# Kernel tuning notes

Measured on AMD Instinct MI355X. Metric: run time of the kernel, lower is better.

The kernel has to match this reference:

```python
import jax, jax.numpy as jnp
import numpy as np

EPS = 1e-6

def gram_schmidt_orthonormalize(U, eps=EPS):
    # U: [B, K, D] -> orthonormalized along K, vectorized over batch
    B, K, D = U.shape
    vs = []
    for i in range(K):
        v = U[:, i]  # [B, D]
        for vj in vs:
            coeff = jnp.sum(v * vj, axis=1, keepdims=True) / (jnp.sum(vj * vj, axis=1, keepdims=True) + eps)
            v = v - coeff * vj
        norm = jnp.maximum(jnp.linalg.norm(v, axis=1, keepdims=True), eps)
        vs.append(v / norm)
    return jnp.stack(vs, axis=1)  # [B, K, D]

def setup_inputs() -> dict:
    key = jax.random.key(0)
    ks = jax.random.split(key, 14)
    B, IN, H1, H2, OUT, E, G = 4096, 1024, 2048, 2048, 512, 8, 256
    s = 0.02
    return {
        "x":   jax.random.normal(ks[0], (B, IN), jnp.float32),
        "W1":  jax.random.normal(ks[1], (E, IN, H1), jnp.float32) * s,
        "b1":  jnp.zeros((E, H1), jnp.float32),
        "W2":  jax.random.normal(ks[2], (E, H1, H2), jnp.float32) * s,
        "b2":  jnp.zeros((E, H2), jnp.float32),
        "W3":  jax.random.normal(ks[3], (E, H2, OUT), jnp.float32) * s,
        "b3":  jnp.zeros((E, OUT), jnp.float32),
        "Wg1": jax.random.normal(ks[4], (IN, G), jnp.float32) * s,
        "bg1": jnp.zeros((G,), jnp.float32),
        "Wg2": jax.random.normal(ks[5], (G, E), jnp.float32) * s,
        "bg2": jnp.zeros((E,), jnp.float32),
        "Wo":  jax.random.normal(ks[6], (OUT, 1), jnp.float32) * s,
        "bo":  jnp.zeros((1,), jnp.float32),
    }

def reference(x, W1, b1, W2, b2, W3, b3, Wg1, bg1, Wg2, bg2, Wo, bo):
    # Expert MLPs, batched over expert axis e: [B,E,h]
    h = jax.nn.relu(jnp.einsum('bi,eih->beh', x, W1) + b1)
    h = jax.nn.relu(jnp.einsum('beh,ehk->bek', h, W2) + b2)
    expert_outputs = jnp.einsum('bek,ekd->bed', h, W3) + b3  # [B, E, D]
    # Gating network: MLP + softmax over experts
    g = jax.nn.relu(x @ Wg1 + bg1)
    gate_weights = jax.nn.softmax(g @ Wg2 + bg2, axis=-1)  # [B, E]
    # Per-sample Gram-Schmidt across experts, weighted combine
    ortho = gram_schmidt_orthonormalize(expert_outputs)  # [B, E, D]
    combined = jnp.einsum('bed,be->bd', ortho, gate_weights)  # [B, D]
    final = combined @ Wo + bo  # [B, 1]
    return (final, 0.0)
```

## Files before the change

### kernel.cpp

```cpp
#include <hip/hip_runtime.h>
#include <hip/hip_bf16.h>

#define DEVINL __device__ __forceinline__

constexpr int Bsz = 4096, INF = 1024, H1 = 2048, H2 = 2048, OUTD = 512, NE = 8, G = 256;

typedef __attribute__((ext_vector_type(8))) short bf16x8;
typedef __attribute__((ext_vector_type(16))) float f32x16;

typedef unsigned short u16;

DEVINL u16 f2bf(float f) {
  unsigned int u = __float_as_uint(f);
  u = (u + 0x7FFFu + ((u >> 16) & 1u)) >> 16;
  return (u16)u;
}
DEVINL float bf2f(u16 h) { return __uint_as_float((unsigned int)h << 16); }

DEVINL void gload16(const void* g, void* l) {
  __builtin_amdgcn_global_load_lds(
      (const __attribute__((address_space(1))) void*)g,
      (__attribute__((address_space(3))) void*)l, 16, 0, 0);
}

DEVINL float waveAllSum(float v) {
#pragma unroll
  for (int m = 32; m > 0; m >>= 1) v += __shfl_xor(v, m, 64);
  return v;
}

DEVINL f32x16 mfma3(bf16x8 bh, bf16x8 bl, bf16x8 ah, bf16x8 al, f32x16 c) {
  c = __builtin_amdgcn_mfma_f32_32x32x16_bf16(bh, ah, c, 0, 0, 0);
  c = __builtin_amdgcn_mfma_f32_32x32x16_bf16(bl, ah, c, 0, 0, 0);
  c = __builtin_amdgcn_mfma_f32_32x32x16_bf16(bh, al, c, 0, 0, 0);
  return c;
}

#define PHASE_MID()                                    \
  __builtin_amdgcn_sched_barrier(0);                   \
  __builtin_amdgcn_s_barrier();                        \
  asm volatile("s_waitcnt lgkmcnt(0)" ::: "memory");   \
  __builtin_amdgcn_sched_barrier(0)
#define PHASE_END()                                    \
  __builtin_amdgcn_sched_barrier(0);                   \
  __builtin_amdgcn_s_barrier()

__global__ __launch_bounds__(256) void pack_act(const float* __restrict__ in,
                                                u16* __restrict__ hi,
                                                u16* __restrict__ lo) {
  size_t i = ((size_t)blockIdx.x * 256 + threadIdx.x) * 4;
  float4 v = *(const float4*)&in[i];
  short4 h, l;
  h.x = f2bf(v.x); l.x = f2bf(v.x - bf2f(h.x));
  h.y = f2bf(v.y); l.y = f2bf(v.y - bf2f(h.y));
  h.z = f2bf(v.z); l.z = f2bf(v.z - bf2f(h.z));
  h.w = f2bf(v.w); l.w = f2bf(v.w - bf2f(h.w));
  *(short4*)&hi[i] = h;
  *(short4*)&lo[i] = l;
}

__global__ __launch_bounds__(256) void pack_wt(const float* __restrict__ W,
                                               u16* __restrict__ Th,
                                               u16* __restrict__ Tl,
                                               int K, int N) {
  __shared__ float t[32][33];
  const int e = blockIdx.z;
  W += (size_t)e * K * N;
  Th += (size_t)e * N * K;
  Tl += (size_t)e * N * K;
  const int n0 = blockIdx.x * 32, k0 = blockIdx.y * 32;
  const int r = threadIdx.x >> 3, c = (threadIdx.x & 7) * 4;
  float4 v = *(const float4*)&W[(size_t)(k0 + r) * N + n0 + c];
  t[r][c + 0] = v.x; t[r][c + 1] = v.y; t[r][c + 2] = v.z; t[r][c + 3] = v.w;
  __syncthreads();
  float o0 = t[c + 0][r], o1 = t[c + 1][r], o2 = t[c + 2][r], o3 = t[c + 3][r];
  short4 h, l;
  h.x = f2bf(o0); l.x = f2bf(o0 - bf2f(h.x));
  h.y = f2bf(o1); l.y = f2bf(o1 - bf2f(h.y));
  h.z = f2bf(o2); l.z = f2bf(o2 - bf2f(h.z));
  h.w = f2bf(o3); l.w = f2bf(o3 - bf2f(h.w));
  *(short4*)&Th[(size_t)(n0 + r) * K + k0 + c] = h;
  *(short4*)&Tl[(size_t)(n0 + r) * K + k0 + c] = l;
}

__global__ __launch_bounds__(512, 2) void gemm32_256(
    const u16* __restrict__ Ahi, const u16* __restrict__ Alo,
    const u16* __restrict__ Bhi, const u16* __restrict__ Blo,
    const float* __restrict__ bias,
    u16* __restrict__ Chi, u16* __restrict__ Clo,
    int M, int N, int K, size_t strideAe) {
  const int e = blockIdx.x;
  Ahi += (size_t)e * strideAe;
  Alo += (size_t)e * strideAe;
  Bhi += (size_t)e * (size_t)N * K;
  Blo += (size_t)e * (size_t)N * K;
  bias += (size_t)e * N;
  Chi += (size_t)e * (size_t)M * N;
  Clo += (size_t)e * (size_t)M * N;

  const int bm = blockIdx.y * 256, bn = blockIdx.z * 256;
  __shared__ __align__(16) char ldsb[131072];
  const int lane = threadIdx.x & 63, wid = threadIdx.x >> 6;
  const int wm = wid >> 2, wn = wid & 3;
  const int l31 = lane & 31, lk = lane >> 5;

  f32x16 acc[4][2];
#pragma unroll
  for (int i = 0; i < 4; ++i)
#pragma unroll
    for (int j = 0; j < 2; ++j)
#pragma unroll
      for (int q = 0; q < 16; ++q) acc[i][j][q] = 0.f;

  const int nt = K / 32;

  auto stageA = [&](const u16* src, int T, int ldsOp) {
    const int s = T & 1;
#pragma unroll
    for (int q = 0; q < 2; ++q) {
      const int g = wid * 2 + q;
      gload16(src + (size_t)(bm + (g >> 1) * 32 + l31) * K + T * 32 + (g & 1) * 16 + lk * 8,
              ldsb + ldsOp + s * 16384 + g * 1024);
    }
  };
  auto stageB = [&](int T, int h) {
    const int s = T & 1;
#pragma unroll
    for (int q = 0; q < 2; ++q) {
      const int g = wid * 2 + q;
      const u16* src = (g < 8) ? Bhi : Blo;
      const int f = g & 7;
      gload16(src + (size_t)(bn + h * 128 + (f >> 1) * 32 + l31) * K + T * 32 + (f & 1) * 16 + lk * 8,
              ldsb + ((g < 8) ? 65536 : 98304) + s * 16384 + h * 8192 + f * 1024);
    }
  };

  bf16x8 ah[2][2], al[2][2], b0h[2], b0l[2], b1h[2], b1l[2];
  auto readA = [&](int s, int ih) {
#pragma unroll
    for (int i = 0; i < 2; ++i)
#pragma unroll
      for (int ks = 0; ks < 2; ++ks) {
        const int off = s * 16384 + ((wm * 4 + ih * 2 + i) * 2 + ks) * 1024 + lane * 16;
        ah[i][ks] = *(const bf16x8*)(ldsb + off);
        al[i][ks] = *(const bf16x8*)(ldsb + 32768 + off);
      }
  };
  auto readB = [&](int s, int jh, bf16x8* bh, bf16x8* bl) {
#pragma unroll
    for (int ks = 0; ks < 2; ++ks) {
      const int off = s * 16384 + ((wn * 2 + jh) * 2 + ks) * 1024 + lane * 16;
      bh[ks] = *(const bf16x8*)(ldsb + 65536 + off);
      bl[ks] = *(const bf16x8*)(ldsb + 98304 + off);
    }
  };

#define QUAD32(IH, JH, BH, BL)                                              \
  __builtin_amdgcn_s_setprio(1);                                            \
  _Pragma("unroll") for (int i = 0; i < 2; ++i) {                           \
    _Pragma("unroll") for (int ks = 0; ks < 2; ++ks) {                      \
      acc[(IH)*2 + i][JH] =                                                 \
          mfma3(BH[ks], BL[ks], ah[i][ks], al[i][ks], acc[(IH)*2 + i][JH]); \
    }                                                                       \
  }                                                                         \
  __builtin_amdgcn_s_setprio(0);

  stageB(0, 0); stageB(0, 1);
  stageA(Ahi, 0, 0); stageA(Alo, 0, 32768);
  stageB(1, 0); stageB(1, 1);
  asm volatile("s_waitcnt vmcnt(4)" ::: "memory");
  __builtin_amdgcn_sched_barrier(0);
  __builtin_amdgcn_s_barrier();

  for (int t = 0; t < nt; ++t) {
    const int s = t & 1;
    readA(s, 0);
    readB(s, 0, b0h, b0l);
    if (t + 1 < nt) stageA(Ahi, t + 1, 0);
    PHASE_MID();
    QUAD32(0, 0, b0h, b0l);
    PHASE_END();
    readB(s, 1, b1h, b1l);
    if (t + 1 < nt) stageA(Alo, t + 1, 32768);
    PHASE_MID();
    QUAD32(0, 1, b1h, b1l);
    PHASE_END();
    readA(s, 1);
    if (t + 2 < nt) stageB(t + 2, 0);
    PHASE_MID();
    QUAD32(1, 0, b0h, b0l);
    PHASE_END();
    if (t + 2 < nt) stageB(t + 2, 1);
    PHASE_MID();
    QUAD32(1, 1, b1h, b1l);
    asm volatile("s_waitcnt vmcnt(4)" ::: "memory");
    __builtin_amdgcn_sched_barrier(0);
    PHASE_END();
  }
#undef QUAD32

#pragma unroll
  for (int rt = 0; rt < 4; ++rt) {
    const int grow = bm + wm * 128 + rt * 32 + l31;
#pragma unroll
    for (int ct = 0; ct < 2; ++ct) {
      const int gcol0 = bn + wn * 64 + ct * 32;
      const f32x16 a = acc[rt][ct];
#pragma unroll
      for (int q = 0; q < 4; ++q) {
        const int c0 = gcol0 + q * 8 + lk * 4;
        const float4 bb = *(const float4*)&bias[c0];
        float v0 = fmaxf(a[q * 4 + 0] + bb.x, 0.f);
        float v1 = fmaxf(a[q * 4 + 1] + bb.y, 0.f);
        float v2 = fmaxf(a[q * 4 + 2] + bb.z, 0.f);
        float v3 = fmaxf(a[q * 4 + 3] + bb.w, 0.f);
        short4 h, l;
        h.x = f2bf(v0); l.x = f2bf(v0 - bf2f(h.x));
        h.y = f2bf(v1); l.y = f2bf(v1 - bf2f(h.y));
        h.z = f2bf(v2); l.z = f2bf(v2 - bf2f(h.z));
        h.w = f2bf(v3); l.w = f2bf(v3 - bf2f(h.w));
        *(short4*)&Chi[(size_t)grow * N + c0] = h;
        *(short4*)&Clo[(size_t)grow * N + c0] = l;
      }
    }
  }
}

__global__ __launch_bounds__(512, 2) void gemm32_128(
    const u16* __restrict__ Ahi, const u16* __restrict__ Alo,
    const u16* __restrict__ Bhi, const u16* __restrict__ Blo,
    const float* __restrict__ bias, float* __restrict__ Cf,
    int M, int N, int K, size_t strideAe) {
  const int e = blockIdx.x;
  Ahi += (size_t)e * strideAe;
  Alo += (size_t)e * strideAe;
  Bhi += (size_t)e * (size_t)N * K;
  Blo += (size_t)e * (size_t)N * K;
  bias += (size_t)e * N;
  Cf += (size_t)e * (size_t)M * N;

  const int bm = blockIdx.y * 128, bn = blockIdx.z * 256;
  __shared__ __align__(16) char ldsb[131072];
  const int lane = threadIdx.x & 63, wid = threadIdx.x >> 6;
  const int wm = wid >> 2, wn = wid & 3;
  const int l31 = lane & 31, lk = lane >> 5;

  f32x16 acc[2][2];
#pragma unroll
  for (int i = 0; i < 2; ++i)
#pragma unroll
    for (int j = 0; j < 2; ++j)
#pragma unroll
      for (int q = 0; q < 16; ++q) acc[i][j][q] = 0.f;

  const int nt = K / 32;

  auto stageA2 = [&](int T) {
    const int s = T & 1;
#pragma unroll
    for (int q = 0; q < 2; ++q) {
      const int g = wid * 2 + q;
      const u16* src = (g < 8) ? Ahi : Alo;
      const int f = g & 7;
      gload16(src + (size_t)(bm + (f >> 1) * 32 + l31) * K + T * 32 + (f & 1) * 16 + lk * 8,
              ldsb + ((g < 8) ? 0 : 16384) + s * 8192 + f * 1024);
    }
  };
  auto stageB2 = [&](int T, int slot) {
#pragma unroll
    for (int q = 0; q < 4; ++q) {
      const int g = wid * 4 + q;
      const u16* src = (g < 16) ? Bhi : Blo;
      const int f = g & 15;
      gload16(src + (size_t)(bn + (f >> 1) * 32 + l31) * K + T * 32 + (f & 1) * 16 + lk * 8,
              ldsb + ((g < 16) ? 32768 : 81920) + slot * 16384 + f * 1024);
    }
  };

  bf16x8 ah[2][2], al[2][2], b0h[2], b0l[2], b1h[2], b1l[2];
  auto readA2 = [&](int s) {
#pragma unroll
    for (int i = 0; i < 2; ++i)
#pragma unroll
      for (int ks = 0; ks < 2; ++ks) {
        const int off = s * 8192 + ((wm * 2 + i) * 2 + ks) * 1024 + lane * 16;
        ah[i][ks] = *(const bf16x8*)(ldsb + off);
        al[i][ks] = *(const bf16x8*)(ldsb + 16384 + off);
      }
  };
  auto readB2 = [&](int bs, int jh, bf16x8* bh, bf16x8* bl) {
#pragma unroll
    for (int ks = 0; ks < 2; ++ks) {
      const int off = bs * 16384 + ((wn * 2 + jh) * 2 + ks) * 1024 + lane * 16;
      bh[ks] = *(const bf16x8*)(ldsb + 32768 + off);
      bl[ks] = *(const bf16x8*)(ldsb + 81920 + off);
    }
  };

#define QUAD2(JH, BH, BL)                                          \
  __builtin_amdgcn_s_setprio(1);                                   \
  _Pragma("unroll") for (int i = 0; i < 2; ++i) {                  \
    _Pragma("unroll") for (int ks = 0; ks < 2; ++ks) {             \
      acc[i][JH] = mfma3(BH[ks], BL[ks], ah[i][ks], al[i][ks], acc[i][JH]); \
    }                                                              \
  }                                                                \
  __builtin_amdgcn_s_setprio(0);

  stageA2(0);
  stageB2(0, 0);
  stageB2(1, 1);
  asm volatile("s_waitcnt vmcnt(4)" ::: "memory");
  __builtin_amdgcn_sched_barrier(0);
  __builtin_amdgcn_s_barrier();

  int bs = 0;
  for (int t = 0; t < nt; ++t) {
    const int sa = t & 1;
    int bs2 = bs - 1; if (bs2 < 0) bs2 = 2;
    readA2(sa);
    readB2(bs, 0, b0h, b0l);
    if (t + 1 < nt) stageA2(t + 1);
    if (t + 2 < nt) stageB2(t + 2, bs2);
    PHASE_MID();
    QUAD2(0, b0h, b0l);
    PHASE_END();
    readB2(bs, 1, b1h, b1l);
    PHASE_MID();
    QUAD2(1, b1h, b1l);
    asm volatile("s_waitcnt vmcnt(4)" ::: "memory");
    __builtin_amdgcn_sched_barrier(0);
    PHASE_END();
    bs = (bs == 2) ? 0 : bs + 1;
  }
#undef QUAD2

#pragma unroll
  for (int rt = 0; rt < 2; ++rt) {
    const int grow = bm + wm * 64 + rt * 32 + l31;
#pragma unroll
    for (int ct = 0; ct < 2; ++ct) {
      const int gcol0 = bn + wn * 64 + ct * 32;
      const f32x16 a = acc[rt][ct];
#pragma unroll
      for (int q = 0; q < 4; ++q) {
        const int c0 = gcol0 + q * 8 + lk * 4;
        const float4 bb = *(const float4*)&bias[c0];
        *(float4*)&Cf[(size_t)grow * N + c0] =
            make_float4(a[q * 4 + 0] + bb.x, a[q * 4 + 1] + bb.y,
                        a[q * 4 + 2] + bb.z, a[q * 4 + 3] + bb.w);
      }
    }
  }
}

__global__ __launch_bounds__(256) void gate1_kernel(
    const float* __restrict__ x, const float* __restrict__ Wg1,
    const float* __restrict__ bg1, float* __restrict__ g) {
  __shared__ float xs[8 * 1024];
  const int b0 = blockIdx.x * 8;
  const float* xp = x + (size_t)b0 * INF;
  for (int idx = threadIdx.x * 4; idx < 8 * 1024; idx += 1024)
    *(float4*)&xs[idx] = *(const float4*)&xp[idx];
  __syncthreads();
  const int t = threadIdx.x;
  float acc[8] = {0, 0, 0, 0, 0, 0, 0, 0};
  for (int i = 0; i < INF; ++i) {
    float w = Wg1[(size_t)i * G + t];
#pragma unroll
    for (int r = 0; r < 8; ++r) acc[r] = fmaf(xs[r * 1024 + i], w, acc[r]);
  }
  const float bb = bg1[t];
#pragma unroll
  for (int r = 0; r < 8; ++r)
    g[(size_t)(b0 + r) * G + t] = fmaxf(acc[r] + bb, 0.0f);
}

__global__ __launch_bounds__(64) void gate2_kernel(
    const float* __restrict__ g, const float* __restrict__ Wg2,
    const float* __restrict__ bg2, float* __restrict__ gw) {
  const int b = blockIdx.x, lane = threadIdx.x;
  float4 gv = *(const float4*)(g + (size_t)b * G + lane * 4);
  float p[8];
#pragma unroll
  for (int e = 0; e < 8; ++e) {
    int j = lane * 4;
    float s = gv.x * Wg2[(j + 0) * 8 + e] + gv.y * Wg2[(j + 1) * 8 + e] +
              gv.z * Wg2[(j + 2) * 8 + e] + gv.w * Wg2[(j + 3) * 8 + e];
    p[e] = waveAllSum(s);
  }
  if (lane == 0) {
    float l[8];
    float mx = -1e30f;
#pragma unroll
    for (int e = 0; e < 8; ++e) {
      l[e] = p[e] + bg2[e];
      mx = fmaxf(mx, l[e]);
    }
    float sum = 0.0f;
#pragma unroll
    for (int e = 0; e < 8; ++e) {
      l[e] = expf(l[e] - mx);
      sum += l[e];
    }
    float inv = 1.0f / sum;
#pragma unroll
    for (int e = 0; e < 8; ++e) gw[(size_t)b * 8 + e] = l[e] * inv;
  }
}

__global__ __launch_bounds__(256) void gs_kernel(
    const float* __restrict__ eo, const float* __restrict__ gw,
    const float* __restrict__ Wo, const float* __restrict__ bo,
    float* __restrict__ out, int CB) {
  const int lane = threadIdx.x & 63;
  const int b = blockIdx.x * 4 + (threadIdx.x >> 6);
  const size_t ES = (size_t)CB * OUTD;
  const float* base = eo + (size_t)b * OUTD + lane * 8;
  float vs[8][8];
  float denom[8];
#pragma unroll
  for (int i = 0; i < 8; ++i) {
    float cur[8];
    float4 u0 = *(const float4*)(base + (size_t)i * ES);
    float4 u1 = *(const float4*)(base + (size_t)i * ES + 4);
    cur[0] = u0.x; cur[1] = u0.y; cur[2] = u0.z; cur[3] = u0.w;
    cur[4] = u1.x; cur[5] = u1.y; cur[6] = u1.z; cur[7] = u1.w;
#pragma unroll
    for (int j = 0; j < i; ++j) {
      float dp = 0.0f;
#pragma unroll
      for (int d = 0; d < 8; ++d) dp = fmaf(cur[d], vs[j][d], dp);
      dp = waveAllSum(dp);
      float coeff = dp / (denom[j] + 1e-6f);
#pragma unroll
      for (int d = 0; d < 8; ++d) cur[d] = fmaf(-coeff, vs[j][d], cur[d]);
    }
    float nn = 0.0f;
#pragma unroll
    for (int d = 0; d < 8; ++d) nn = fmaf(cur[d], cur[d], nn);
    nn = waveAllSum(nn);
    float inv = 1.0f / fmaxf(sqrtf(nn), 1e-6f);
#pragma unroll
    for (int d = 0; d < 8; ++d) vs[i][d] = cur[d] * inv;
    float dd = 0.0f;
#pragma unroll
    for (int d = 0; d < 8; ++d) dd = fmaf(vs[i][d], vs[i][d], dd);
    denom[i] = waveAllSum(dd);
  }
  float gwv[8];
#pragma unroll
  for (int e = 0; e < 8; ++e) gwv[e] = gw[(size_t)b * 8 + e];
  float part = 0.0f;
#pragma unroll
  for (int d = 0; d < 8; ++d) {
    float c = 0.0f;
#pragma unroll
    for (int e = 0; e < 8; ++e) c = fmaf(vs[e][d], gwv[e], c);
    part = fmaf(c, Wo[lane * 8 + d], part);
  }
  part = waveAllSum(part);
  if (lane == 0) out[b] = part + bo[0];
}

extern "C" void kernel_launch(void* const* d_in, const int* in_sizes, int n_in,
                              void* d_out, int out_size, void* d_ws, size_t ws_size,
                              hipStream_t stream) {
  const float* x   = (const float*)d_in[0];
  const float* W1  = (const float*)d_in[1];
  const float* b1  = (const float*)d_in[2];
  const float* W2  = (const float*)d_in[3];
  const float* b2  = (const float*)d_in[4];
  const float* W3  = (const float*)d_in[5];
  const float* b3  = (const float*)d_in[6];
  const float* Wg1 = (const float*)d_in[7];
  const float* bg1 = (const float*)d_in[8];
  const float* Wg2 = (const float*)d_in[9];
  const float* bg2 = (const float*)d_in[10];
  const float* Wo  = (const float*)d_in[11];
  const float* bo  = (const float*)d_in[12];
  float* out = (float*)d_out;

  char* p = (char*)d_ws;
  float* gw = (float*)p;          p += (size_t)(128u << 10);
  float* g  = (float*)p;          p += (size_t)(4u << 20);
  u16* xhi = (u16*)p;             p += (size_t)Bsz * INF * 2;
  u16* xlo = (u16*)p;             p += (size_t)Bsz * INF * 2;
  u16* w1h = (u16*)p;             p += (size_t)NE * H1 * INF * 2;
  u16* w1l = (u16*)p;             p += (size_t)NE * H1 * INF * 2;
  u16* w2h = (u16*)p;             p += (size_t)NE * H2 * H1 * 2;
  u16* w2l = (u16*)p;             p += (size_t)NE * H2 * H1 * 2;
  u16* w3h = (u16*)p;             p += (size_t)NE * OUTD * H2 * 2;
  u16* w3l = (u16*)p;             p += (size_t)NE * OUTD * H2 * 2;
  const size_t fixedBytes = (size_t)(p - (char*)d_ws);

  int CB = 4096;
  while (CB > 256 && fixedBytes + (size_t)CB * (size_t)(128u << 10) > ws_size) CB >>= 1;
  u16* h1h = (u16*)p;
  u16* h1l = h1h + (size_t)NE * CB * H1;
  u16* h2h = h1l + (size_t)NE * CB * H1;
  u16* h2l = h2h + (size_t)NE * CB * H2;
  float* eo = (float*)h1h;

  hipMemsetAsync(d_out, 0, (size_t)out_size * sizeof(float), stream);

  pack_act<<<(Bsz * INF) / 1024, 256, 0, stream>>>(x, xhi, xlo);
  pack_wt<<<dim3(H1 / 32, INF / 32, NE), 256, 0, stream>>>(W1, w1h, w1l, INF, H1);
  pack_wt<<<dim3(H2 / 32, H1 / 32, NE), 256, 0, stream>>>(W2, w2h, w2l, H1, H2);
  pack_wt<<<dim3(OUTD / 32, H2 / 32, NE), 256, 0, stream>>>(W3, w3h, w3l, H2, OUTD);

  gate1_kernel<<<Bsz / 8, 256, 0, stream>>>(x, Wg1, bg1, g);
  gate2_kernel<<<Bsz, 64, 0, stream>>>(g, Wg2, bg2, gw);

  for (int c0 = 0; c0 < Bsz; c0 += CB) {
    gemm32_256<<<dim3(NE, CB / 256, H1 / 256), 512, 0, stream>>>(
        xhi + (size_t)c0 * INF, xlo + (size_t)c0 * INF, w1h, w1l, b1,
        h1h, h1l, CB, H1, INF, (size_t)0);
    gemm32_256<<<dim3(NE, CB / 256, H2 / 256), 512, 0, stream>>>(
        h1h, h1l, w2h, w2l, b2, h2h, h2l, CB, H2, H1, (size_t)CB * H1);
    gemm32_128<<<dim3(NE, CB / 128, OUTD / 256), 512, 0, stream>>>(
        h2h, h2l, w3h, w3l, b3, eo, CB, OUTD, H2, (size_t)CB * H2);
    gs_kernel<<<CB / 4, 256, 0, stream>>>(eo, gw + (size_t)c0 * NE, Wo, bo,
                                          out + c0, CB);
  }
}
```

Baseline: 1.888 ms.

## Switch big expert GEMMs to 16x16x32 MFMA tiles with two-barrier pipeline

```diff
diff --git a/kernel.cpp b/kernel.cpp
--- a/kernel.cpp
+++ b/kernel.cpp
@@ -6,8 +6,8 @@
 constexpr int Bsz = 4096, INF = 1024, H1 = 2048, H2 = 2048, OUTD = 512, NE = 8, G = 256;
 
 typedef __attribute__((ext_vector_type(8))) short bf16x8;
+typedef __attribute__((ext_vector_type(4))) float f32x4;
 typedef __attribute__((ext_vector_type(16))) float f32x16;
-
 typedef unsigned short u16;
 
 DEVINL u16 f2bf(float f) {
@@ -83,7 +83,7 @@
   *(short4*)&Tl[(size_t)(n0 + r) * K + k0 + c] = l;
 }
 
-__global__ __launch_bounds__(512, 2) void gemm32_256(
+__global__ __launch_bounds__(512, 2) void gemm_2bar(
     const u16* __restrict__ Ahi, const u16* __restrict__ Alo,
     const u16* __restrict__ Bhi, const u16* __restrict__ Blo,
     const float* __restrict__ bias,
@@ -102,15 +102,14 @@
   __shared__ __align__(16) char ldsb[131072];
   const int lane = threadIdx.x & 63, wid = threadIdx.x >> 6;
   const int wm = wid >> 2, wn = wid & 3;
-  const int l31 = lane & 31, lk = lane >> 5;
-
-  f32x16 acc[4][2];
-#pragma unroll
-  for (int i = 0; i < 4; ++i)
-#pragma unroll
-    for (int j = 0; j < 2; ++j)
-#pragma unroll
-      for (int q = 0; q < 16; ++q) acc[i][j][q] = 0.f;
+  const int l15 = lane & 15, l4 = lane >> 4;
+  const int bhalf = wn >> 1, jn = wn & 1;
+
+  f32x4 acc[8][4];
+#pragma unroll
+  for (int i = 0; i < 8; ++i)
+#pragma unroll
+    for (int j = 0; j < 4; ++j) acc[i][j] = (f32x4){0.f, 0.f, 0.f, 0.f};
 
   const int nt = K / 32;
 
@@ -119,7 +118,7 @@
 #pragma unroll
     for (int q = 0; q < 2; ++q) {
       const int g = wid * 2 + q;
-      gload16(src + (size_t)(bm + (g >> 1) * 32 + l31) * K + T * 32 + (g & 1) * 16 + lk * 8,
+      gload16(src + (size_t)(bm + g * 16 + l15) * K + T * 32 + l4 * 8,
               ldsb + ldsOp + s * 16384 + g * 1024);
     }
   };
@@ -130,39 +129,40 @@
       const int g = wid * 2 + q;
       const u16* src = (g < 8) ? Bhi : Blo;
       const int f = g & 7;
-      gload16(src + (size_t)(bn + h * 128 + (f >> 1) * 32 + l31) * K + T * 32 + (f & 1) * 16 + lk * 8,
+      gload16(src + (size_t)(bn + h * 128 + f * 16 + l15) * K + T * 32 + l4 * 8,
               ldsb + ((g < 8) ? 65536 : 98304) + s * 16384 + h * 8192 + f * 1024);
     }
   };
 
-  bf16x8 ah[2][2], al[2][2], b0h[2], b0l[2], b1h[2], b1l[2];
+  bf16x8 ah[4], al[4], bh[4], bl[4];
   auto readA = [&](int s, int ih) {
 #pragma unroll
-    for (int i = 0; i < 2; ++i)
-#pragma unroll
-      for (int ks = 0; ks < 2; ++ks) {
-        const int off = s * 16384 + ((wm * 4 + ih * 2 + i) * 2 + ks) * 1024 + lane * 16;
-        ah[i][ks] = *(const bf16x8*)(ldsb + off);
-        al[i][ks] = *(const bf16x8*)(ldsb + 32768 + off);
-      }
-  };
-  auto readB = [&](int s, int jh, bf16x8* bh, bf16x8* bl) {
-#pragma unroll
-    for (int ks = 0; ks < 2; ++ks) {
-      const int off = s * 16384 + ((wn * 2 + jh) * 2 + ks) * 1024 + lane * 16;
-      bh[ks] = *(const bf16x8*)(ldsb + 65536 + off);
-      bl[ks] = *(const bf16x8*)(ldsb + 98304 + off);
-    }
-  };
-
-#define QUAD32(IH, JH, BH, BL)                                              \
-  __builtin_amdgcn_s_setprio(1);                                            \
-  _Pragma("unroll") for (int i = 0; i < 2; ++i) {                           \
-    _Pragma("unroll") for (int ks = 0; ks < 2; ++ks) {                      \
-      acc[(IH)*2 + i][JH] =                                                 \
-          mfma3(BH[ks], BL[ks], ah[i][ks], al[i][ks], acc[(IH)*2 + i][JH]); \
-    }                                                                       \
-  }                                                                         \
+    for (int i = 0; i < 4; ++i) {
+      const int off = s * 16384 + wm * 8192 + (ih * 4 + i) * 1024 + lane * 16;
+      ah[i] = *(const bf16x8*)(ldsb + off);
+      al[i] = *(const bf16x8*)(ldsb + 32768 + off);
+    }
+  };
+  auto readBall = [&](int s) {
+#pragma unroll
+    for (int j = 0; j < 4; ++j) {
+      const int off = s * 16384 + bhalf * 8192 + (jn * 4 + j) * 1024 + lane * 16;
+      bh[j] = *(const bf16x8*)(ldsb + 65536 + off);
+      bl[j] = *(const bf16x8*)(ldsb + 98304 + off);
+    }
+  };
+
+#define QUAD48(IH)                                                             \
+  __builtin_amdgcn_s_setprio(1);                                               \
+  _Pragma("unroll") for (int i = 0; i < 4; ++i) {                              \
+    _Pragma("unroll") for (int j = 0; j < 4; ++j) {                            \
+      f32x4 a = acc[(IH)*4 + i][j];                                            \
+      a = __builtin_amdgcn_mfma_f32_16x16x32_bf16(bh[j], ah[i], a, 0, 0, 0);   \
+      a = __builtin_amdgcn_mfma_f32_16x16x32_bf16(bl[j], ah[i], a, 0, 0, 0);   \
+      a = __builtin_amdgcn_mfma_f32_16x16x32_bf16(bh[j], al[i], a, 0, 0, 0);   \
+      acc[(IH)*4 + i][j] = a;                                                  \
+    }                                                                          \
+  }                                                                            \
   __builtin_amdgcn_s_setprio(0);
 
   stageB(0, 0); stageB(0, 1);
@@ -175,53 +175,43 @@
   for (int t = 0; t < nt; ++t) {
     const int s = t & 1;
     readA(s, 0);
-    readB(s, 0, b0h, b0l);
-    if (t + 1 < nt) stageA(Ahi, t + 1, 0);
-    PHASE_MID();
-    QUAD32(0, 0, b0h, b0l);
-    PHASE_END();
-    readB(s, 1, b1h, b1l);
-    if (t + 1 < nt) stageA(Alo, t + 1, 32768);
-    PHASE_MID();
-    QUAD32(0, 1, b1h, b1l);
-    PHASE_END();
+    readBall(s);
+    if (t + 1 < nt) { stageA(Ahi, t + 1, 0); stageA(Alo, t + 1, 32768); }
+    asm volatile("s_waitcnt lgkmcnt(0)" ::: "memory");
+    __builtin_amdgcn_sched_barrier(0);
+    QUAD48(0);
+    __builtin_amdgcn_sched_barrier(0);
+    __builtin_amdgcn_s_barrier();
     readA(s, 1);
-    if (t + 2 < nt) stageB(t + 2, 0);
-    PHASE_MID();
-    QUAD32(1, 0, b0h, b0l);
-    PHASE_END();
-    if (t + 2 < nt) stageB(t + 2, 1);
-    PHASE_MID();
-    QUAD32(1, 1, b1h, b1l);
-    asm volatile("s_waitcnt vmcnt(4)" ::: "memory");
+    if (t + 2 < nt) { stageB(t + 2, 0); stageB(t + 2, 1); }
+    asm volatile("s_waitcnt lgkmcnt(0)" ::: "memory");
     __builtin_amdgcn_sched_barrier(0);
-    PHASE_END();
-  }
-#undef QUAD32
-
-#pragma unroll
-  for (int rt = 0; rt < 4; ++rt) {
-    const int grow = bm + wm * 128 + rt * 32 + l31;
-#pragma unroll
-    for (int ct = 0; ct < 2; ++ct) {
-      const int gcol0 = bn + wn * 64 + ct * 32;
-      const f32x16 a = acc[rt][ct];
-#pragma unroll
-      for (int q = 0; q < 4; ++q) {
-        const int c0 = gcol0 + q * 8 + lk * 4;
-        const float4 bb = *(const float4*)&bias[c0];
-        float v0 = fmaxf(a[q * 4 + 0] + bb.x, 0.f);
-        float v1 = fmaxf(a[q * 4 + 1] + bb.y, 0.f);
-        float v2 = fmaxf(a[q * 4 + 2] + bb.z, 0.f);
-        float v3 = fmaxf(a[q * 4 + 3] + bb.w, 0.f);
-        short4 h, l;
-        h.x = f2bf(v0); l.x = f2bf(v0 - bf2f(h.x));
-        h.y = f2bf(v1); l.y = f2bf(v1 - bf2f(h.y));
-        h.z = f2bf(v2); l.z = f2bf(v2 - bf2f(h.z));
-        h.w = f2bf(v3); l.w = f2bf(v3 - bf2f(h.w));
-        *(short4*)&Chi[(size_t)grow * N + c0] = h;
-        *(short4*)&Clo[(size_t)grow * N + c0] = l;
-      }
+    QUAD48(1);
+    if (t + 2 < nt) { asm volatile("s_waitcnt vmcnt(4)" ::: "memory"); }
+    else            { asm volatile("s_waitcnt vmcnt(0)" ::: "memory"); }
+    __builtin_amdgcn_sched_barrier(0);
+    __builtin_amdgcn_s_barrier();
+  }
+#undef QUAD48
+
+#pragma unroll
+  for (int i = 0; i < 8; ++i) {
+    const int grow = bm + wm * 128 + i * 16 + l15;
+#pragma unroll
+    for (int j = 0; j < 4; ++j) {
+      const int gcol = bn + wn * 64 + j * 16 + l4 * 4;
+      const float4 bb = *(const float4*)&bias[gcol];
+      float v0 = fmaxf(acc[i][j][0] + bb.x, 0.f);
+      float v1 = fmaxf(acc[i][j][1] + bb.y, 0.f);
+      float v2 = fmaxf(acc[i][j][2] + bb.z, 0.f);
+      float v3 = fmaxf(acc[i][j][3] + bb.w, 0.f);
+      short4 h, l;
+      h.x = f2bf(v0); l.x = f2bf(v0 - bf2f(h.x));
+      h.y = f2bf(v1); l.y = f2bf(v1 - bf2f(h.y));
+      h.z = f2bf(v2); l.z = f2bf(v2 - bf2f(h.z));
+      h.w = f2bf(v3); l.w = f2bf(v3 - bf2f(h.w));
+      *(short4*)&Chi[(size_t)grow * N + gcol] = h;
+      *(short4*)&Clo[(size_t)grow * N + gcol] = l;
     }
   }
 }
@@ -297,13 +287,13 @@
     }
   };
 
-#define QUAD2(JH, BH, BL)                                          \
-  __builtin_amdgcn_s_setprio(1);                                   \
-  _Pragma("unroll") for (int i = 0; i < 2; ++i) {                  \
-    _Pragma("unroll") for (int ks = 0; ks < 2; ++ks) {             \
+#define QUAD2(JH, BH, BL)                                                   \
+  __builtin_amdgcn_s_setprio(1);                                            \
+  _Pragma("unroll") for (int i = 0; i < 2; ++i) {                           \
+    _Pragma("unroll") for (int ks = 0; ks < 2; ++ks) {                      \
       acc[i][JH] = mfma3(BH[ks], BL[ks], ah[i][ks], al[i][ks], acc[i][JH]); \
-    }                                                              \
-  }                                                                \
+    }                                                                       \
+  }                                                                         \
   __builtin_amdgcn_s_setprio(0);
 
   stageA2(0);
@@ -327,7 +317,8 @@
     readB2(bs, 1, b1h, b1l);
     PHASE_MID();
     QUAD2(1, b1h, b1l);
-    asm volatile("s_waitcnt vmcnt(4)" ::: "memory");
+    if (t + 2 < nt) { asm volatile("s_waitcnt vmcnt(4)" ::: "memory"); }
+    else            { asm volatile("s_waitcnt vmcnt(0)" ::: "memory"); }
     __builtin_amdgcn_sched_barrier(0);
     PHASE_END();
     bs = (bs == 2) ? 0 : bs + 1;
@@ -512,10 +503,10 @@
   gate2_kernel<<<Bsz, 64, 0, stream>>>(g, Wg2, bg2, gw);
 
   for (int c0 = 0; c0 < Bsz; c0 += CB) {
-    gemm32_256<<<dim3(NE, CB / 256, H1 / 256), 512, 0, stream>>>(
+    gemm_2bar<<<dim3(NE, CB / 256, H1 / 256), 512, 0, stream>>>(
         xhi + (size_t)c0 * INF, xlo + (size_t)c0 * INF, w1h, w1l, b1,
         h1h, h1l, CB, H1, INF, (size_t)0);
-    gemm32_256<<<dim3(NE, CB / 256, H2 / 256), 512, 0, stream>>>(
+    gemm_2bar<<<dim3(NE, CB / 256, H2 / 256), 512, 0, stream>>>(
         h1h, h1l, w2h, w2l, b2, h2h, h2l, CB, H2, H1, (size_t)CB * H1);
     gemm32_128<<<dim3(NE, CB / 128, OUTD / 256), 512, 0, stream>>>(
         h2h, h2l, w3h, w3l, b3, eo, CB, OUTD, H2, (size_t)CB * H2);
```

Result: faster. 1.585 ms (-16.0%).
